# Kernel tuning notes

Measured on AMD Instinct MI355X. Metric: run time of the kernel, lower is better.

Reference implementation:

```python
import jax, jax.numpy as jnp
import numpy as np

MAX_BITS = 8   # codes are stored at 8 bits (max of supported_bits), 4 codes per int32
W_BITS = 4     # active bit-width -> lut has 2**W_BITS entries per output row


def setup_inputs() -> dict:
    key = jax.random.key(0)
    k1, k2, k3 = jax.random.split(key, 3)
    B, S = 1, 2048
    OUT, IN = 8192, 8192
    x = jax.random.normal(k1, (B, S, IN), dtype=jnp.float32)
    qweight = jax.random.randint(k2, (OUT, IN // 4), 0, 2147483647, dtype=jnp.int32)
    # per-output-channel lookup table for w_bits=4 -> 16 entries
    lut = jax.random.normal(k3, (OUT, 2 ** W_BITS), dtype=jnp.float32)
    return {"x": x, "qweight": qweight, "lut": lut}


def dequant_kbit(qweight, lut, w_bits):
    # qweight: (O, K//4) int32 -> 8-bit codes (O, K)
    O = qweight.shape[0]
    shifts = jnp.array([0, 8, 16, 24], dtype=jnp.int32)
    codes = (qweight[:, :, None] >> shifts) & 0xFF          # (O, K//4, 4)
    codes = codes.reshape(O, -1)                             # (O, K)
    # any-precision: top w_bits of the 8-bit code index the w_bits LUT
    idx = codes >> (MAX_BITS - w_bits)                       # (O, K) in [0, 2**w_bits)
    weight = jnp.take_along_axis(lut, idx, axis=1)           # (O, K)
    return weight


def reference(x, qweight, lut):
    # bulk path of AnyprecisionLinear.forward (tokens > 8): dequant then matmul
    weight = dequant_kbit(qweight, lut, W_BITS)              # (O, K)
    out = jnp.einsum('bsk,ok->bso', x, weight)               # (B, S, O)
    return out
```

## Files before the change

### kernel.cpp

```cpp
#include <hip/hip_runtime.h>
#include <stdint.h>


#define M_DIM 2048
#define N_DIM 8192
#define K_DIM 8192
#define BM 256
#define BN 256
#define BK 64
#define KT (K_DIM / BK)

typedef __bf16 bf16x8 __attribute__((ext_vector_type(8)));
typedef float f32x4 __attribute__((ext_vector_type(4)));

__device__ __forceinline__ unsigned int f2bf(float f) {
  unsigned int u = __float_as_uint(f);
  return (u + 0x7FFFu + ((u >> 16) & 1u)) >> 16;
}

__global__ __launch_bounds__(256) void dequant_kernel(
    const int4* __restrict__ qw4,
    const float* __restrict__ lut,
    unsigned short* __restrict__ wb) {
  __shared__ unsigned int slut[4 * 16 * 64];
  const int wave = threadIdx.x >> 6;
  const int lane = threadIdx.x & 63;
  const int row = (blockIdx.x << 2) + wave;

  unsigned int* tbl = slut + wave * (16 * 64) + lane;
  const float* lr = lut + row * 16;
#pragma unroll
  for (int e = 0; e < 16; ++e) tbl[e * 64] = f2bf(lr[e]);

  const int4* src = qw4 + (size_t)row * 512 + lane;
  unsigned short* dst = wb + (size_t)row * K_DIM + lane * 16;

#pragma unroll
  for (int it = 0; it < 8; ++it) {
    int4 q = src[it * 64];
    unsigned int w[4] = {(unsigned int)q.x, (unsigned int)q.y,
                         (unsigned int)q.z, (unsigned int)q.w};
    unsigned int v[16];
#pragma unroll
    for (int j = 0; j < 4; ++j) {
#pragma unroll
      for (int k = 0; k < 4; ++k)
        v[j * 4 + k] = tbl[((w[j] >> (8 * k + 4)) & 15u) * 64];
    }
    uint4 o0, o1;
    o0.x = v[0] | (v[1] << 16);   o0.y = v[2]  | (v[3] << 16);
    o0.z = v[4] | (v[5] << 16);   o0.w = v[6]  | (v[7] << 16);
    o1.x = v[8] | (v[9] << 16);   o1.y = v[10] | (v[11] << 16);
    o1.z = v[12] | (v[13] << 16); o1.w = v[14] | (v[15] << 16);
    uint4* dp = (uint4*)(dst + it * 1024);
    dp[0] = o0;
    dp[1] = o1;
  }
}

__global__ __launch_bounds__(256) void cvt_x_kernel(
    const float4* __restrict__ x4, unsigned int* __restrict__ xb) {
  const int idx = blockIdx.x * 256 + threadIdx.x;
  float4 a = x4[2 * idx];
  float4 b = x4[2 * idx + 1];
  uint4 o;
  o.x = f2bf(a.x) | (f2bf(a.y) << 16);
  o.y = f2bf(a.z) | (f2bf(a.w) << 16);
  o.z = f2bf(b.x) | (f2bf(b.y) << 16);
  o.w = f2bf(b.z) | (f2bf(b.w) << 16);
  ((uint4*)xb)[idx] = o;
}


__device__ __forceinline__ void stage_q(const unsigned short* __restrict__ g,
                                        unsigned short* lds_tile, int grow0,
                                        int qrow, int koff, int wave, int srow,
                                        int scol) {
  const unsigned short* src =
      g + (size_t)(grow0 + qrow + (wave << 3) + srow) * K_DIM + koff + scol;
  __builtin_amdgcn_global_load_lds(
      (const __attribute__((address_space(1))) void*)src,
      (__attribute__((address_space(3))) void*)(lds_tile +
                                                (qrow + (wave << 3)) * BK),
      16, 0, 0);
}

__device__ __forceinline__ void load_a4(const unsigned short* __restrict__ s,
                                        int row0, int rrow, int rk,
                                        bf16x8 out[4][2]) {
#pragma unroll
  for (int mi = 0; mi < 4; ++mi) {
    const int row = row0 + mi * 16 + rrow;
    const int sw = row & 7;
#pragma unroll
    for (int ks = 0; ks < 2; ++ks) {
      const int slot = (ks * 4 + rk) ^ sw;
      out[mi][ks] = *(const bf16x8*)(s + row * BK + slot * 8);
    }
  }
}

__device__ __forceinline__ void load_b2(const unsigned short* __restrict__ s,
                                        int row0, int rrow, int rk,
                                        bf16x8 out[2][2]) {
#pragma unroll
  for (int nj = 0; nj < 2; ++nj) {
    const int row = row0 + nj * 16 + rrow;
    const int sw = row & 7;
#pragma unroll
    for (int ks = 0; ks < 2; ++ks) {
      const int slot = (ks * 4 + rk) ^ sw;
      out[nj][ks] = *(const bf16x8*)(s + row * BK + slot * 8);
    }
  }
}

#define MFMA_Q(AH, BH)                                                        \
  _Pragma("unroll")                                                           \
  for (int ks = 0; ks < 2; ++ks)                                              \
    _Pragma("unroll")                                                         \
    for (int mi = 0; mi < 4; ++mi)                                            \
      _Pragma("unroll")                                                       \
      for (int nj = 0; nj < 2; ++nj)                                          \
        acc[(AH)*4 + mi][(BH)*2 + nj] =                                       \
            __builtin_amdgcn_mfma_f32_16x16x32_bf16(                          \
                af[mi][ks], bq[nj][ks], acc[(AH)*4 + mi][(BH)*2 + nj], 0, 0, 0);

#define SBAR asm volatile("s_barrier" ::: "memory")

#define KTILE(T, BF)                                                          \
  {                                                                           \
    const int ko1 = (((T) + 1) & (KT - 1)) * BK;                              \
    const int ko2 = (((T) + 2) & (KT - 1)) * BK;                              \
    const unsigned short* sa_ = sA[BF];                                       \
    const unsigned short* sb_ = sB[BF];                                       \
    unsigned short* naB = sB[(BF) ^ 1];                                       \
    unsigned short* caA = sA[BF];                                             \
    unsigned short* caB = sB[BF];                                             \
                                                          \
    load_a4(sa_, wm + 0, rrow, rk, af);                                       \
    load_b2(sb_, bnlo, rrow, rk, bq);                                         \
    stage_q(B, naB, n0, 0, ko1, wave, srow, scol);                            \
    stage_q(B, naB, n0, 64, ko1, wave, srow, scol);                           \
    asm volatile("s_waitcnt lgkmcnt(8)" ::: "memory");                        \
    SBAR;                                                                     \
    __builtin_amdgcn_s_setprio(1);                                            \
    MFMA_Q(0, 0);                                                             \
    __builtin_amdgcn_s_setprio(0);                                            \
    SBAR;                                                                     \
                                               \
    load_b2(sb_, bnlo + 128, rrow, rk, bq);                                   \
    stage_q(A, caA, m0, 0, ko2, wave, srow, scol);                            \
    stage_q(A, caA, m0, 128, ko2, wave, srow, scol);                          \
    SBAR;                                                                     \
    __builtin_amdgcn_s_setprio(1);                                            \
    MFMA_Q(0, 1);                                                             \
    __builtin_amdgcn_s_setprio(0);                                            \
    SBAR;                                                                     \
                                               \
    load_a4(sa_, wm + 64, rrow, rk, af);                                      \
    stage_q(B, caB, n0, 128, ko2, wave, srow, scol);                          \
    stage_q(B, caB, n0, 192, ko2, wave, srow, scol);                          \
    SBAR;                                                                     \
    __builtin_amdgcn_s_setprio(1);                                            \
    MFMA_Q(1, 1);                                                             \
    __builtin_amdgcn_s_setprio(0);                                            \
    SBAR;                                                                     \
                                               \
    load_b2(sb_, bnlo, rrow, rk, bq);                                         \
    stage_q(A, caA, m0, 64, ko2, wave, srow, scol);                           \
    stage_q(A, caA, m0, 192, ko2, wave, srow, scol);                          \
    SBAR;                                                                     \
    __builtin_amdgcn_s_setprio(1);                                            \
    MFMA_Q(1, 0);                                                             \
    __builtin_amdgcn_s_setprio(0);                                            \
    asm volatile("s_waitcnt vmcnt(6)" ::: "memory");                          \
    SBAR;                                                                     \
  }

__global__ __launch_bounds__(512, 2) void gemm_bt(
    const unsigned short* __restrict__ A,
    const unsigned short* __restrict__ B,
    float* __restrict__ C) {
  __shared__ __align__(16) unsigned short sA[2][BM * BK];
  __shared__ __align__(16) unsigned short sB[2][BN * BK];

  const int tid = threadIdx.x;
  const int wave = tid >> 6;
  const int lane = tid & 63;

  const int bid = blockIdx.x;
  const int swz = (bid & 7) * 32 + (bid >> 3);
  const int m0 = (swz >> 5) * BM;
  const int n0 = (swz & 31) * BN;

  const int wm = (wave >> 2) * 128;
  const int bnlo = (wave & 3) * 32;

  const int srow = lane >> 3;
  const int scol = ((lane & 7) ^ srow) * 8;

  const int rrow = lane & 15;
  const int rk = lane >> 4;

  bf16x8 af[4][2];
  bf16x8 bq[2][2];
  f32x4 acc[8][4];
#pragma unroll
  for (int m = 0; m < 8; ++m)
#pragma unroll
    for (int n = 0; n < 4; ++n)
#pragma unroll
      for (int r = 0; r < 4; ++r) acc[m][n][r] = 0.0f;

  stage_q(A, sA[0], m0, 0, 0, wave, srow, scol);
  stage_q(A, sA[0], m0, 64, 0, wave, srow, scol);
  stage_q(A, sA[0], m0, 128, 0, wave, srow, scol);
  stage_q(A, sA[0], m0, 192, 0, wave, srow, scol);
  stage_q(B, sB[0], n0, 0, 0, wave, srow, scol);
  stage_q(B, sB[0], n0, 64, 0, wave, srow, scol);
  stage_q(B, sB[0], n0, 128, 0, wave, srow, scol);
  stage_q(B, sB[0], n0, 192, 0, wave, srow, scol);
  stage_q(A, sA[1], m0, 0, BK, wave, srow, scol);
  stage_q(A, sA[1], m0, 128, BK, wave, srow, scol);
  stage_q(B, sB[1], n0, 128, BK, wave, srow, scol);
  stage_q(B, sB[1], n0, 192, BK, wave, srow, scol);
  stage_q(A, sA[1], m0, 64, BK, wave, srow, scol);
  stage_q(A, sA[1], m0, 192, BK, wave, srow, scol);
  asm volatile("s_waitcnt vmcnt(6)" ::: "memory");
  SBAR;

#pragma unroll 1
  for (int tt = 0; tt < KT / 2; ++tt) {
    KTILE(2 * tt, 0)
    KTILE(2 * tt + 1, 1)
  }
  asm volatile("s_waitcnt vmcnt(0)" ::: "memory");

  const int crow0 = m0 + wm + 4 * rk;
  const int ccol0 = n0 + bnlo + rrow;
#pragma unroll
  for (int m = 0; m < 8; ++m)
#pragma unroll
    for (int n = 0; n < 4; ++n)
#pragma unroll
      for (int r = 0; r < 4; ++r)
        C[(size_t)(crow0 + m * 16 + r) * N_DIM + ccol0 + (n >> 1) * 128 +
          (n & 1) * 16] = acc[m][n][r];
}

__global__ void naive_kernel(const float* __restrict__ x,
                             const int* __restrict__ qw,
                             const float* __restrict__ lut,
                             float* __restrict__ out) {
  int o = blockIdx.x * blockDim.x + threadIdx.x;
  int s = blockIdx.y;
  const float* xr = x + (size_t)s * K_DIM;
  const unsigned int* qr = (const unsigned int*)qw + (size_t)o * (K_DIM / 4);
  const float* l = lut + o * 16;
  float acc = 0.f;
  for (int w = 0; w < K_DIM / 4; ++w) {
    unsigned int q = qr[w];
    acc += xr[w * 4 + 0] * l[(q >> 4) & 15u]
         + xr[w * 4 + 1] * l[(q >> 12) & 15u]
         + xr[w * 4 + 2] * l[(q >> 20) & 15u]
         + xr[w * 4 + 3] * l[(q >> 28) & 15u];
  }
  out[(size_t)s * N_DIM + o] = acc;
}

extern "C" void kernel_launch(void* const* d_in, const int* in_sizes, int n_in,
                              void* d_out, int out_size, void* d_ws,
                              size_t ws_size, hipStream_t stream) {
  const float* x = (const float*)d_in[0];
  const int* qw = (const int*)d_in[1];
  const float* lut = (const float*)d_in[2];
  float* out = (float*)d_out;

  const size_t wb_elems = (size_t)N_DIM * K_DIM;
  const size_t xb_elems = (size_t)M_DIM * K_DIM;
  const size_t need = (wb_elems + xb_elems) * sizeof(unsigned short);

  if (ws_size >= need) {
    unsigned short* wb = (unsigned short*)d_ws;
    unsigned short* xb = wb + wb_elems;

    hipLaunchKernelGGL(dequant_kernel, dim3(N_DIM / 4), dim3(256), 0, stream,
                       (const int4*)qw, lut, wb);

    const int n_thr = M_DIM * K_DIM / 8;
    hipLaunchKernelGGL(cvt_x_kernel, dim3(n_thr / 256), dim3(256), 0, stream,
                       (const float4*)x, (unsigned int*)xb);

    hipLaunchKernelGGL(gemm_bt, dim3((M_DIM / BM) * (N_DIM / BN)), dim3(512),
                       0, stream, xb, wb, out);
  } else {
    dim3 grid(N_DIM / 256, M_DIM);
    hipLaunchKernelGGL(naive_kernel, grid, dim3(256), 0, stream, x, qw, lut,
                       out);
  }
}
```

Before: 453.2 us.

## Double-buffer MFMA register fragments and prefetch next tile's fragments across K-tiles

Restructures the K-tile loop so A/B fragment registers are double-buffered (afA/afB, bqA/bqB). The first fragments of the next K-tile are now loaded during the current tile's last quarters, which removes the LDS-read wait at the start of each tile and drops one barrier per quarter. Swizzled LDS offsets are precomputed once per thread instead of recomputed in every load. The prologue now stages both full tiles up front. The cost is higher VGPR pressure from the doubled fragments, which could hurt at launch bounds of 512 threads with 2 blocks per CU, and more fragile ordering between barriers and waitcnts.

```diff
diff --git a/kernel.cpp b/kernel.cpp
--- a/kernel.cpp
+++ b/kernel.cpp
@@ -86,95 +86,82 @@
 }
 
 __device__ __forceinline__ void load_a4(const unsigned short* __restrict__ s,
-                                        int row0, int rrow, int rk,
+                                        int row0, int aoff0, int aoff1,
                                         bf16x8 out[4][2]) {
 #pragma unroll
   for (int mi = 0; mi < 4; ++mi) {
-    const int row = row0 + mi * 16 + rrow;
-    const int sw = row & 7;
-#pragma unroll
-    for (int ks = 0; ks < 2; ++ks) {
-      const int slot = (ks * 4 + rk) ^ sw;
-      out[mi][ks] = *(const bf16x8*)(s + row * BK + slot * 8);
-    }
+    out[mi][0] = *(const bf16x8*)(s + (row0 + mi * 16) * BK + aoff0);
+    out[mi][1] = *(const bf16x8*)(s + (row0 + mi * 16) * BK + aoff1);
   }
 }
 
 __device__ __forceinline__ void load_b2(const unsigned short* __restrict__ s,
-                                        int row0, int rrow, int rk,
+                                        int row0, int aoff0, int aoff1,
                                         bf16x8 out[2][2]) {
 #pragma unroll
   for (int nj = 0; nj < 2; ++nj) {
-    const int row = row0 + nj * 16 + rrow;
-    const int sw = row & 7;
-#pragma unroll
-    for (int ks = 0; ks < 2; ++ks) {
-      const int slot = (ks * 4 + rk) ^ sw;
-      out[nj][ks] = *(const bf16x8*)(s + row * BK + slot * 8);
-    }
-  }
-}
-
-#define MFMA_Q(AH, BH)                                                        \
+    out[nj][0] = *(const bf16x8*)(s + (row0 + nj * 16) * BK + aoff0);
+    out[nj][1] = *(const bf16x8*)(s + (row0 + nj * 16) * BK + aoff1);
+  }
+}
+
+#define MFMA_Q(AF, BQ, MH, NH)                                                \
   _Pragma("unroll")                                                           \
   for (int ks = 0; ks < 2; ++ks)                                              \
     _Pragma("unroll")                                                         \
     for (int mi = 0; mi < 4; ++mi)                                            \
       _Pragma("unroll")                                                       \
       for (int nj = 0; nj < 2; ++nj)                                          \
-        acc[(AH)*4 + mi][(BH)*2 + nj] =                                       \
+        acc[(MH)*4 + mi][(NH)*2 + nj] =                                       \
             __builtin_amdgcn_mfma_f32_16x16x32_bf16(                          \
-                af[mi][ks], bq[nj][ks], acc[(AH)*4 + mi][(BH)*2 + nj], 0, 0, 0);
+                AF[mi][ks], BQ[nj][ks], acc[(MH)*4 + mi][(NH)*2 + nj],        \
+                0, 0, 0);
 
 #define SBAR asm volatile("s_barrier" ::: "memory")
 
 #define KTILE(T, BF)                                                          \
   {                                                                           \
-    const int ko1 = (((T) + 1) & (KT - 1)) * BK;                              \
     const int ko2 = (((T) + 2) & (KT - 1)) * BK;                              \
     const unsigned short* sa_ = sA[BF];                                       \
     const unsigned short* sb_ = sB[BF];                                       \
-    unsigned short* naB = sB[(BF) ^ 1];                                       \
-    unsigned short* caA = sA[BF];                                             \
-    unsigned short* caB = sB[BF];                                             \
-                                                          \
-    load_a4(sa_, wm + 0, rrow, rk, af);                                       \
-    load_b2(sb_, bnlo, rrow, rk, bq);                                         \
-    stage_q(B, naB, n0, 0, ko1, wave, srow, scol);                            \
-    stage_q(B, naB, n0, 64, ko1, wave, srow, scol);                           \
-    asm volatile("s_waitcnt lgkmcnt(8)" ::: "memory");                        \
-    SBAR;                                                                     \
-    __builtin_amdgcn_s_setprio(1);                                            \
-    MFMA_Q(0, 0);                                                             \
-    __builtin_amdgcn_s_setprio(0);                                            \
-    SBAR;                                                                     \
-                                               \
-    load_b2(sb_, bnlo + 128, rrow, rk, bq);                                   \
-    stage_q(A, caA, m0, 0, ko2, wave, srow, scol);                            \
-    stage_q(A, caA, m0, 128, ko2, wave, srow, scol);                          \
-    SBAR;                                                                     \
-    __builtin_amdgcn_s_setprio(1);                                            \
-    MFMA_Q(0, 1);                                                             \
-    __builtin_amdgcn_s_setprio(0);                                            \
-    SBAR;                                                                     \
-                                               \
-    load_a4(sa_, wm + 64, rrow, rk, af);                                      \
-    stage_q(B, caB, n0, 128, ko2, wave, srow, scol);                          \
-    stage_q(B, caB, n0, 192, ko2, wave, srow, scol);                          \
-    SBAR;                                                                     \
-    __builtin_amdgcn_s_setprio(1);                                            \
-    MFMA_Q(1, 1);                                                             \
-    __builtin_amdgcn_s_setprio(0);                                            \
-    SBAR;                                                                     \
-                                               \
-    load_b2(sb_, bnlo, rrow, rk, bq);                                         \
-    stage_q(A, caA, m0, 64, ko2, wave, srow, scol);                           \
-    stage_q(A, caA, m0, 192, ko2, wave, srow, scol);                          \
-    SBAR;                                                                     \
-    __builtin_amdgcn_s_setprio(1);                                            \
-    MFMA_Q(1, 0);                                                             \
-    __builtin_amdgcn_s_setprio(0);                                            \
-    asm volatile("s_waitcnt vmcnt(6)" ::: "memory");                          \
+    const unsigned short* sa1 = sA[(BF) ^ 1];                                 \
+    const unsigned short* sb1 = sB[(BF) ^ 1];                                 \
+    unsigned short* wa = sA[BF];                                              \
+    unsigned short* wbuf = sB[BF];                                            \
+                          \
+    load_b2(sb_, bnlo + 128, aoff0, aoff1, bqB);                              \
+    stage_q(A, wa, m0, 0, ko2, wave, srow, scol);                             \
+    stage_q(A, wa, m0, 128, ko2, wave, srow, scol);                           \
+    __builtin_amdgcn_s_setprio(1);                                            \
+    MFMA_Q(afA, bqA, 0, 0);                                                   \
+    __builtin_amdgcn_s_setprio(0);                                            \
+    SBAR;                                                                     \
+                          \
+    load_a4(sa_, wm + 64, aoff0, aoff1, afB);                                 \
+    stage_q(B, wbuf, n0, 0, ko2, wave, srow, scol);                           \
+    stage_q(B, wbuf, n0, 64, ko2, wave, srow, scol);                          \
+    __builtin_amdgcn_s_setprio(1);                                            \
+    MFMA_Q(afA, bqB, 0, 1);                                                   \
+    __builtin_amdgcn_s_setprio(0);                                            \
+    asm volatile("s_waitcnt lgkmcnt(0)" ::: "memory");                        \
+    SBAR;                                                                     \
+         \
+    load_a4(sa1, wm + 0, aoff0, aoff1, afA);                                  \
+    stage_q(A, wa, m0, 64, ko2, wave, srow, scol);                            \
+    stage_q(A, wa, m0, 192, ko2, wave, srow, scol);                           \
+    __builtin_amdgcn_s_setprio(1);                                            \
+    MFMA_Q(afB, bqA, 1, 0);                                                   \
+    __builtin_amdgcn_s_setprio(0);                                            \
+    SBAR;                                                                     \
+         \
+    load_b2(sb1, bnlo, aoff0, aoff1, bqA);                                    \
+    stage_q(B, wbuf, n0, 128, ko2, wave, srow, scol);                         \
+    stage_q(B, wbuf, n0, 192, ko2, wave, srow, scol);                         \
+    __builtin_amdgcn_s_setprio(1);                                            \
+    MFMA_Q(afB, bqB, 1, 1);                                                   \
+    __builtin_amdgcn_s_setprio(0);                                            \
+    asm volatile("s_waitcnt lgkmcnt(0)" ::: "memory");                        \
+    asm volatile("s_waitcnt vmcnt(8)" ::: "memory");                          \
     SBAR;                                                                     \
   }
 
@@ -202,9 +189,11 @@
 
   const int rrow = lane & 15;
   const int rk = lane >> 4;
-
-  bf16x8 af[4][2];
-  bf16x8 bq[2][2];
+  const int aoff0 = rrow * BK + ((rk) ^ (rrow & 7)) * 8;
+  const int aoff1 = rrow * BK + ((4 + rk) ^ (rrow & 7)) * 8;
+
+  bf16x8 afA[4][2], afB[4][2];
+  bf16x8 bqA[2][2], bqB[2][2];
   f32x4 acc[8][4];
 #pragma unroll
   for (int m = 0; m < 8; ++m)
@@ -222,12 +211,18 @@
   stage_q(B, sB[0], n0, 128, 0, wave, srow, scol);
   stage_q(B, sB[0], n0, 192, 0, wave, srow, scol);
   stage_q(A, sA[1], m0, 0, BK, wave, srow, scol);
+  stage_q(A, sA[1], m0, 64, BK, wave, srow, scol);
   stage_q(A, sA[1], m0, 128, BK, wave, srow, scol);
+  stage_q(A, sA[1], m0, 192, BK, wave, srow, scol);
+  stage_q(B, sB[1], n0, 0, BK, wave, srow, scol);
+  stage_q(B, sB[1], n0, 64, BK, wave, srow, scol);
   stage_q(B, sB[1], n0, 128, BK, wave, srow, scol);
   stage_q(B, sB[1], n0, 192, BK, wave, srow, scol);
-  stage_q(A, sA[1], m0, 64, BK, wave, srow, scol);
-  stage_q(A, sA[1], m0, 192, BK, wave, srow, scol);
-  asm volatile("s_waitcnt vmcnt(6)" ::: "memory");
+  asm volatile("s_waitcnt vmcnt(8)" ::: "memory");
+  SBAR;
+  load_a4(sA[0], wm + 0, aoff0, aoff1, afA);
+  load_b2(sB[0], bnlo, aoff0, aoff1, bqA);
+  asm volatile("s_waitcnt lgkmcnt(0)" ::: "memory");
   SBAR;
 
 #pragma unroll 1
@@ -235,7 +230,7 @@
     KTILE(2 * tt, 0)
     KTILE(2 * tt + 1, 1)
   }
-  asm volatile("s_waitcnt vmcnt(0)" ::: "memory");
+  asm volatile("s_waitcnt vmcnt(0) lgkmcnt(0)" ::: "memory");
 
   const int crow0 = m0 + wm + 4 * rk;
   const int ccol0 = n0 + bnlo + rrow;
```

Result: slower. 535.4 us (+18.2%).
